# Kernel tuning notes

Hardware: AMD Instinct MI355X
Metric: run time of the kernel (lower is better)

Reference implementation:

```python
import jax, jax.numpy as jnp
import numpy as np

N = 16384      # total ligand atoms
E = 65536      # edges
B = 256        # graphs / batch
MAXN = 64      # atoms per graph (max_nodes for to_dense_batch)
FIN = 64       # num_node_features
HID = 256      # hidden_channels
GH = 2         # gat heads
LP = 1024      # protein length
NH = 4         # cross-attention heads
HD = HID // NH
VOCAB = 22


def setup_inputs() -> dict:
    key = jax.random.key(0)
    ks = jax.random.split(key, 48)
    f = jnp.float32
    def nrm(k, shape, s=0.05):
        return jax.random.normal(k, shape, f) * s
    inp = {}
    inp["x"] = jax.random.normal(ks[0], (N, FIN), f)
    inp["edge_index"] = jax.random.randint(ks[1], (2, E), 0, N)
    inp["batch"] = jnp.arange(N) // MAXN  # sorted, 64 atoms per graph
    inp["protein_seq"] = jax.random.randint(ks[2], (B, LP), 0, VOCAB)
    # GAT layer 1 (FIN -> HID, GH heads, concat=False)
    inp["w1"] = nrm(ks[3], (FIN, GH * HID)); inp["as1"] = nrm(ks[4], (GH, HID)); inp["ad1"] = nrm(ks[5], (GH, HID)); inp["b1"] = jnp.zeros((HID,), f)
    inp["w2"] = nrm(ks[6], (HID, GH * HID)); inp["as2"] = nrm(ks[7], (GH, HID)); inp["ad2"] = nrm(ks[8], (GH, HID)); inp["b2"] = jnp.zeros((HID,), f)
    inp["w3"] = nrm(ks[9], (HID, GH * HID)); inp["as3"] = nrm(ks[10], (GH, HID)); inp["ad3"] = nrm(ks[11], (GH, HID)); inp["b3"] = jnp.zeros((HID,), f)
    # protein embedding + conv1d (OIH layout)
    inp["emb"] = nrm(ks[12], (VOCAB, HID), 0.1)
    inp["conv_w"] = nrm(ks[13], (HID, HID, 3)); inp["conv_b"] = jnp.zeros((HID,), f)
    # cross-attention MHA
    inp["wq"] = nrm(ks[14], (HID, HID)); inp["bq"] = jnp.zeros((HID,), f)
    inp["wk"] = nrm(ks[15], (HID, HID)); inp["bk"] = jnp.zeros((HID,), f)
    inp["wv"] = nrm(ks[16], (HID, HID)); inp["bv"] = jnp.zeros((HID,), f)
    inp["wo"] = nrm(ks[17], (HID, HID)); inp["bo"] = jnp.zeros((HID,), f)
    inp["ln1_g"] = jnp.ones((HID,), f); inp["ln1_b"] = jnp.zeros((HID,), f)
    inp["ffw1"] = nrm(ks[18], (HID, 4 * HID)); inp["ffb1"] = jnp.zeros((4 * HID,), f)
    inp["ffw2"] = nrm(ks[19], (4 * HID, HID)); inp["ffb2"] = jnp.zeros((HID,), f)
    inp["ln2_g"] = jnp.ones((HID,), f); inp["ln2_b"] = jnp.zeros((HID,), f)
    inp["fc1_w"] = nrm(ks[20], (HID, HID)); inp["fc1_b"] = jnp.zeros((HID,), f)
    inp["fc2_w"] = nrm(ks[21], (HID, 1)); inp["fc2_b"] = jnp.zeros((1,), f)
    return inp


def _gat(x, edge_index, W, a_src, a_dst, bias):
    # PyG GATConv, concat=False (mean over heads), add_self_loops=True
    n = x.shape[0]
    h = (x @ W).reshape(n, GH, HID)                      # [N,GH,C]
    loop = jnp.arange(n)
    src = jnp.concatenate([edge_index[0], loop])
    dst = jnp.concatenate([edge_index[1], loop])
    a_s = jnp.einsum('nhc,hc->nh', h, a_src)             # [N,GH]
    a_d = jnp.einsum('nhc,hc->nh', h, a_dst)
    e = jax.nn.leaky_relu(a_s[src] + a_d[dst], 0.2)      # [E+N,GH]
    emax = jax.ops.segment_max(e, dst, num_segments=n)   # each node has a self-loop
    ex = jnp.exp(e - emax[dst])
    den = jax.ops.segment_sum(ex, dst, num_segments=n)
    alpha = ex / den[dst]                                # [E+N,GH]
    msg = h[src] * alpha[:, :, None]
    out = jax.ops.segment_sum(msg, dst, num_segments=n)  # [N,GH,C]
    return out.mean(axis=1) + bias


def _to_dense_batch(x, batch):
    # batch is sorted node->graph ids; counts per graph <= MAXN
    ones = jnp.ones((x.shape[0],), jnp.int32)
    counts = jax.ops.segment_sum(ones, batch, num_segments=B)
    starts = jnp.cumsum(counts) - counts
    pos = jnp.arange(x.shape[0]) - starts[batch]
    dense = jnp.zeros((B, MAXN, x.shape[1]), x.dtype).at[batch, pos].set(x)
    mask = jnp.zeros((B, MAXN), bool).at[batch, pos].set(True)
    return dense, mask


def _layernorm(x, g, b, eps=1e-5):
    mu = x.mean(-1, keepdims=True)
    var = ((x - mu) ** 2).mean(-1, keepdims=True)
    return (x - mu) * jax.lax.rsqrt(var + eps) * g + b


def reference(x, edge_index, batch, protein_seq,
              w1, as1, ad1, b1, w2, as2, ad2, b2, w3, as3, ad3, b3,
              emb, conv_w, conv_b,
              wq, bq, wk, bk, wv, bv, wo, bo,
              ln1_g, ln1_b, ffw1, ffb1, ffw2, ffb2, ln2_g, ln2_b,
              fc1_w, fc1_b, fc2_w, fc2_b):
    # --- ligand GNN (eval mode: dropout = identity) ---
    h = jax.nn.elu(_gat(x, edge_index, w1, as1, ad1, b1))
    h = jax.nn.elu(_gat(h, edge_index, w2, as2, ad2, b2))
    h = jax.nn.elu(_gat(h, edge_index, w3, as3, ad3, b3))
    lig, lig_mask = _to_dense_batch(h, batch)            # [B,MAXN,HID], [B,MAXN]
    # --- protein branch ---
    p = emb[protein_seq]                                 # [B,LP,HID]
    p = p.transpose(0, 2, 1)                             # [B,HID,LP]
    p = jax.lax.conv_general_dilated(p, conv_w, (1,), [(1, 1)],
                                     dimension_numbers=('NCH', 'OIH', 'NCH'))
    p = jax.nn.relu(p + conv_b[None, :, None]).transpose(0, 2, 1)  # [B,LP,HID]
    kpm = protein_seq == 0                               # key padding mask
    # --- cross attention (query=ligand, key/value=protein) ---
    q = (lig @ wq + bq).reshape(B, MAXN, NH, HD)
    k = (p @ wk + bk).reshape(B, LP, NH, HD)
    v = (p @ wv + bv).reshape(B, LP, NH, HD)
    scores = jnp.einsum('bqhd,bkhd->bhqk', q, k) / np.sqrt(HD).astype(np.float32)
    scores = jnp.where(kpm[:, None, None, :], jnp.float32(-1e9), scores)
    attn = jax.nn.softmax(scores, axis=-1)               # [B,NH,MAXN,LP]
    ctx = jnp.einsum('bhqk,bkhd->bqhd', attn, v).reshape(B, MAXN, HID)
    attn_out = ctx @ wo + bo
    y = _layernorm(lig + attn_out, ln1_g, ln1_b)
    ff = jax.nn.gelu(y @ ffw1 + ffb1, approximate=False) @ ffw2 + ffb2
    y = _layernorm(y + ff, ln2_g, ln2_b)
    # --- masked mean pool ---
    m = lig_mask[:, :, None].astype(y.dtype)
    pooled = (y * m).sum(axis=1) / (m.sum(axis=1) + 1e-6)
    out = jax.nn.relu(pooled @ fc1_w + fc1_b)
    return out @ fc2_w + fc2_b                           # [B,1]
```

## Files before the change

### kernel.cpp

```cpp
#include <hip/hip_runtime.h>
#include <hip/hip_bf16.h>
#include <cstdint>
#include <cstddef>

#define NAT 16384
#define NED 65536
#define BGR 256
#define FIN 64
#define HID 256
#define LPN 1024
#define HD 64
#define NTRIP 11638
#define NTAB  11648

typedef __bf16 bf16x8 __attribute__((ext_vector_type(8)));
typedef float floatx4 __attribute__((ext_vector_type(4)));

__device__ __forceinline__ void gl2lds16(const void* g, void* l)
{
    __builtin_amdgcn_global_load_lds(
        (const __attribute__((address_space(1))) unsigned int*)g,
        (__attribute__((address_space(3))) unsigned int*)l, 16, 0, 0);
}

template<int ACT, int OUTBF16, int BIASROW, int HSPLIT>
__global__ __launch_bounds__(512) void gemm_mfma(const __bf16* __restrict__ A,
    const __bf16* __restrict__ Bt, const float* __restrict__ bias,
    void* __restrict__ Cout, int M, int Nn, int K, float escale)
{
    __shared__ __bf16 As[2][128][32];
    __shared__ __bf16 Bs[2][128][32];
    const int t = threadIdx.x;
    const int m0 = blockIdx.y * 128, n0 = blockIdx.x * 128;
    const int w = t >> 6, lane = t & 63;
    const int wm = (w & 3) * 32, wn = (w >> 2) * 64;
    const int quad = lane >> 4, l16 = lane & 15;
    const int r0 = t >> 2, s0 = t & 3, g0 = (s0 ^ (r0 & 3)) * 8;
    const int fso = (quad ^ (l16 & 3)) * 8;
    floatx4 acc[2][4] = {};
    for (int k0 = 0; k0 < K; k0 += 64) {
        gl2lds16(A + (size_t)(m0 + r0) * K + k0 + g0,       &As[0][r0][s0 * 8]);
        gl2lds16(A + (size_t)(m0 + r0) * K + k0 + 32 + g0,  &As[1][r0][s0 * 8]);
        gl2lds16(Bt + (size_t)(n0 + r0) * K + k0 + g0,      &Bs[0][r0][s0 * 8]);
        gl2lds16(Bt + (size_t)(n0 + r0) * K + k0 + 32 + g0, &Bs[1][r0][s0 * 8]);
        __syncthreads();
#pragma unroll
        for (int c = 0; c < 2; c++) {
            bf16x8 af[2], bfr[4];
#pragma unroll
            for (int mi = 0; mi < 2; mi++) af[mi]  = *(const bf16x8*)&As[c][wm + mi * 16 + l16][fso];
#pragma unroll
            for (int nj = 0; nj < 4; nj++) bfr[nj] = *(const bf16x8*)&Bs[c][wn + nj * 16 + l16][fso];
#pragma unroll
            for (int mi = 0; mi < 2; mi++)
#pragma unroll
                for (int nj = 0; nj < 4; nj++)
                    acc[mi][nj] = __builtin_amdgcn_mfma_f32_16x16x32_bf16(af[mi], bfr[nj], acc[mi][nj], 0, 0, 0);
        }
        __syncthreads();
    }
#pragma unroll
    for (int mi = 0; mi < 2; mi++)
#pragma unroll
        for (int nj = 0; nj < 4; nj++) {
            int col = n0 + wn + nj * 16 + l16;
#pragma unroll
            for (int r = 0; r < 4; r++) {
                int row = m0 + wm + mi * 16 + quad * 4 + r;
                float bval = bias ? (BIASROW ? bias[row] : bias[col]) : 0.f;
                float v = (acc[mi][nj][r] + bval) * escale;
                if (ACT == 1) v = fmaxf(v, 0.f);
                if (ACT == 2) v = 0.5f * v * (1.f + erff(v * 0.70710678118654752f));
                if (HSPLIT)      ((__bf16*)Cout)[((size_t)(col >> 6) * M + row) * 64 + (col & 63)] = (__bf16)v;
                else if (OUTBF16) ((__bf16*)Cout)[(size_t)row * Nn + col] = (__bf16)v;
                else              ((float*)Cout)[(size_t)row * Nn + col] = v;
            }
        }
}

__global__ __launch_bounds__(512) void ffn_k(const __bf16* __restrict__ A,
    const __bf16* __restrict__ W1t, const __bf16* __restrict__ W2t,
    const float* __restrict__ b1, const float* __restrict__ b2,
    float* __restrict__ Cout)
{
    __shared__ __bf16 As[64 * 256];
    __shared__ __bf16 Hs[64 * 128];
    const int t = threadIdx.x;
    const int m0 = blockIdx.x * 64;
    const int w = t >> 6, lane = t & 63;
    const int rg = w & 1, cg = w >> 1;
    const int quad = lane >> 4, l16 = lane & 15;
#pragma unroll
    for (int it = 0; it < 4; it++) {
        const int idx = it * 512 + t;
        const int row = idx >> 5, cs = idx & 31;
        const int c = (cs & 24) | ((cs & 7) ^ (row & 7));
        gl2lds16(A + (size_t)(m0 + row) * 256 + c * 8, &As[idx * 8]);
    }
    floatx4 acc2[2][4] = {};
    __syncthreads();
    const int arow0 = rg * 32 + l16;
    for (int ch = 0; ch < 8; ch++) {
        floatx4 acc1[2][2] = {};
#pragma unroll
        for (int w32 = 0; w32 < 8; w32++) {
            bf16x8 a[2];
#pragma unroll
            for (int mi = 0; mi < 2; mi++) {
                const int row = arow0 + mi * 16;
                const int c = w32 * 4 + quad;
                const int slot = (c & 24) | ((c & 7) ^ (row & 7));
                a[mi] = *(const bf16x8*)&As[row * 256 + slot * 8];
            }
#pragma unroll
            for (int nj = 0; nj < 2; nj++) {
                const int hcol = ch * 128 + cg * 32 + nj * 16 + l16;
                bf16x8 bfrag = *(const bf16x8*)(W1t + (size_t)hcol * 256 + w32 * 32 + quad * 8);
#pragma unroll
                for (int mi = 0; mi < 2; mi++)
                    acc1[mi][nj] = __builtin_amdgcn_mfma_f32_16x16x32_bf16(a[mi], bfrag, acc1[mi][nj], 0, 0, 0);
            }
        }
#pragma unroll
        for (int nj = 0; nj < 2; nj++) {
            const int col = cg * 32 + nj * 16 + l16;
            const float bv = b1[ch * 128 + col];
            const int ch8 = col >> 3;
#pragma unroll
            for (int mi = 0; mi < 2; mi++)
#pragma unroll
                for (int r = 0; r < 4; r++) {
                    const int row = rg * 32 + mi * 16 + quad * 4 + r;
                    float v = acc1[mi][nj][r] + bv;
                    v = 0.5f * v * (1.f + erff(v * 0.70710678118654752f));
                    const int slot = (ch8 & 8) | ((ch8 & 7) ^ (row & 7));
                    Hs[row * 128 + slot * 8 + (col & 7)] = (__bf16)v;
                }
        }
        __syncthreads();
#pragma unroll
        for (int ks = 0; ks < 4; ks++) {
            bf16x8 a[2];
#pragma unroll
            for (int mi = 0; mi < 2; mi++) {
                const int row = arow0 + mi * 16;
                const int c8 = ks * 4 + quad;
                const int slot = (c8 & 8) | ((c8 & 7) ^ (row & 7));
                a[mi] = *(const bf16x8*)&Hs[row * 128 + slot * 8];
            }
#pragma unroll
            for (int nj = 0; nj < 4; nj++) {
                const int ocol = cg * 64 + nj * 16 + l16;
                bf16x8 bfrag = *(const bf16x8*)(W2t + (size_t)ocol * 1024 + ch * 128 + ks * 32 + quad * 8);
#pragma unroll
                for (int mi = 0; mi < 2; mi++)
                    acc2[mi][nj] = __builtin_amdgcn_mfma_f32_16x16x32_bf16(a[mi], bfrag, acc2[mi][nj], 0, 0, 0);
            }
        }
        __syncthreads();
    }
#pragma unroll
    for (int mi = 0; mi < 2; mi++)
#pragma unroll
        for (int nj = 0; nj < 4; nj++) {
            const int col = cg * 64 + nj * 16 + l16;
            const float bv = b2[col];
#pragma unroll
            for (int r = 0; r < 4; r++) {
                const int row = m0 + rg * 32 + mi * 16 + quad * 4 + r;
                Cout[(size_t)row * 256 + col] = acc2[mi][nj][r] + bv;
            }
        }
}

__global__ __launch_bounds__(512) void gemm_gat(const __bf16* __restrict__ A,
    const __bf16* __restrict__ Bt, const float* __restrict__ as_f,
    const float* __restrict__ ad_f, __bf16* __restrict__ Hg,
    float* __restrict__ part, int K)
{
    __shared__ __bf16 As[2][128][32];
    __shared__ __bf16 Bs[2][128][32];
    const int t = threadIdx.x;
    const int m0 = blockIdx.y * 128, n0 = blockIdx.x * 128;
    const int w = t >> 6, lane = t & 63;
    const int wm = (w & 3) * 32, wn = (w >> 2) * 64;
    const int quad = lane >> 4, l16 = lane & 15;
    const int r0 = t >> 2, s0 = t & 3, g0 = (s0 ^ (r0 & 3)) * 8;
    const int fso = (quad ^ (l16 & 3)) * 8;
    floatx4 acc[2][4] = {};
    for (int k0 = 0; k0 < K; k0 += 64) {
        gl2lds16(A + (size_t)(m0 + r0) * K + k0 + g0,       &As[0][r0][s0 * 8]);
        gl2lds16(A + (size_t)(m0 + r0) * K + k0 + 32 + g0,  &As[1][r0][s0 * 8]);
        gl2lds16(Bt + (size_t)(n0 + r0) * K + k0 + g0,      &Bs[0][r0][s0 * 8]);
        gl2lds16(Bt + (size_t)(n0 + r0) * K + k0 + 32 + g0, &Bs[1][r0][s0 * 8]);
        __syncthreads();
#pragma unroll
        for (int c = 0; c < 2; c++) {
            bf16x8 af[2], bfr[4];
#pragma unroll
            for (int mi = 0; mi < 2; mi++) af[mi]  = *(const bf16x8*)&As[c][wm + mi * 16 + l16][fso];
#pragma unroll
            for (int nj = 0; nj < 4; nj++) bfr[nj] = *(const bf16x8*)&Bs[c][wn + nj * 16 + l16][fso];
#pragma unroll
            for (int mi = 0; mi < 2; mi++)
#pragma unroll
                for (int nj = 0; nj < 4; nj++)
                    acc[mi][nj] = __builtin_amdgcn_mfma_f32_16x16x32_bf16(af[mi], bfr[nj], acc[mi][nj], 0, 0, 0);
        }
        __syncthreads();
    }
    const int slot = blockIdx.x * 2 + (w >> 2);
#pragma unroll
    for (int mi = 0; mi < 2; mi++) {
#pragma unroll
        for (int r = 0; r < 4; r++) {
            float ps = 0.f, pd = 0.f;
#pragma unroll
            for (int nj = 0; nj < 4; nj++) {
                int col = n0 + wn + nj * 16 + l16;
                float v = acc[mi][nj][r];
                ps += v * as_f[col];
                pd += v * ad_f[col];
            }
#pragma unroll
            for (int off = 1; off < 16; off <<= 1) {
                ps += __shfl_xor(ps, off, 64);
                pd += __shfl_xor(pd, off, 64);
            }
            if (l16 == 0) {
                int row = m0 + wm + mi * 16 + quad * 4 + r;
                part[(size_t)(slot * 2 + 0) * NAT + row] = ps;
                part[(size_t)(slot * 2 + 1) * NAT + row] = pd;
            }
        }
    }
#pragma unroll
    for (int mi = 0; mi < 2; mi++)
#pragma unroll
        for (int nj = 0; nj < 4; nj++) {
            int col = n0 + wn + nj * 16 + l16;
#pragma unroll
            for (int r = 0; r < 4; r++) {
                int row = m0 + wm + mi * 16 + quad * 4 + r;
                Hg[(size_t)row * 512 + col] = (__bf16)acc[mi][nj][r];
            }
        }
}

__global__ void fold_k(const float* __restrict__ part, float* __restrict__ a_s,
                       float* __restrict__ a_d)
{
    int n = blockIdx.x * 256 + threadIdx.x;
    float s0 = 0.f, d0 = 0.f, s1 = 0.f, d1 = 0.f;
#pragma unroll
    for (int sl = 0; sl < 4; sl++) {
        s0 += part[(size_t)(sl * 2 + 0) * NAT + n];
        d0 += part[(size_t)(sl * 2 + 1) * NAT + n];
        s1 += part[(size_t)((sl + 4) * 2 + 0) * NAT + n];
        d1 += part[(size_t)((sl + 4) * 2 + 1) * NAT + n];
    }
    a_s[n * 2 + 0] = s0; a_s[n * 2 + 1] = s1;
    a_d[n * 2 + 0] = d0; a_d[n * 2 + 1] = d1;
}

__global__ __launch_bounds__(256) void tap_k(const float* __restrict__ emb,
    const float* __restrict__ cw, float* __restrict__ tap)
{
    const int dlv = blockIdx.x >> 2, part = blockIdx.x & 3;
    const int dl = dlv / 22, v = dlv % 22;
    const int n = threadIdx.x;
    const float* er = emb + v * 256 + part * 64;
    const float* wr = cw + (size_t)n * 768 + part * 192 + dl;
    float s = 0.f;
    for (int k = 0; k < 64; k += 4) {
        s += er[k + 0] * wr[k * 3 + 0];
        s += er[k + 1] * wr[k * 3 + 3];
        s += er[k + 2] * wr[k * 3 + 6];
        s += er[k + 3] * wr[k * 3 + 9];
    }
    atomicAdd(&tap[(size_t)dlv * 256 + n], s);
}

__global__ __launch_bounds__(256) void ptab_k(const float* __restrict__ tap,
    const float* __restrict__ bias, __bf16* __restrict__ P)
{
    const int t = threadIdx.x;
    const int row = blockIdx.x * 8 + (t >> 5);
    const int c = (t & 31) * 8;
    __bf16 o[8];
    if (row < NTRIP) {
        const int a = row / 506, rem = row - a * 506;
        const int t1 = rem / 23, c2 = rem - t1 * 23;
        float acc[8];
#pragma unroll
        for (int j = 0; j < 8; j++) acc[j] = bias[c + j];
        if (a > 0) {
            const float* r = tap + (size_t)(0 * 22 + (a - 1)) * 256 + c;
#pragma unroll
            for (int j = 0; j < 8; j++) acc[j] += r[j];
        }
        {
            const float* r = tap + (size_t)(1 * 22 + t1) * 256 + c;
#pragma unroll
            for (int j = 0; j < 8; j++) acc[j] += r[j];
        }
        if (c2 > 0) {
            const float* r = tap + (size_t)(2 * 22 + (c2 - 1)) * 256 + c;
#pragma unroll
            for (int j = 0; j < 8; j++) acc[j] += r[j];
        }
#pragma unroll
        for (int j = 0; j < 8; j++) o[j] = (__bf16)fmaxf(acc[j], 0.f);
    } else {
#pragma unroll
        for (int j = 0; j < 8; j++) o[j] = (__bf16)0.f;
    }
    *(uint4*)(P + (size_t)row * 256 + c) = *(uint4*)o;
}

__global__ void tid_k(const int* __restrict__ seq, unsigned short* __restrict__ tid)
{
    int i = blockIdx.x * 256 + threadIdx.x;
    int b = i >> 10, l = i & 1023;
    const int* sr = seq + b * LPN;
    int t0 = (l > 0) ? sr[l - 1] : -1;
    int t1 = sr[l];
    int t2 = (l < LPN - 1) ? sr[l + 1] : -1;
    int v = (t0 + 1) * 506 + t1 * 23 + (t2 + 1);
    tid[i] = (unsigned short)(v | (t1 == 0 ? 0x8000 : 0));
}

struct Segs {
    const float* src[12];
    __bf16* dst[12];
    int kdim[12];
    int ndim[12];
    int mode[12];
    int start[13];
};

__global__ void cvtall_k(Segs S, int total)
{
    int i = blockIdx.x * 256 + threadIdx.x;
    if (i >= total) return;
    int s = 0;
    while (i >= S.start[s + 1]) s++;
    int j = i - S.start[s];
    if (S.mode[s] == 0) {
        S.dst[s][j] = (__bf16)S.src[s][j];
    } else {
        int K = S.kdim[s], N = S.ndim[s];
        int n = j / K, k = j - n * K;
        S.dst[s][j] = (__bf16)S.src[s][(size_t)k * N + n];
    }
}

__global__ void deg_k(const int* __restrict__ ei, int* __restrict__ deg)
{
    int e = blockIdx.x * 256 + threadIdx.x;
    if (e < NED) atomicAdd(&deg[ei[NED + e]], 1);
}

__global__ __launch_bounds__(256) void scan_k(const int* __restrict__ deg, int* __restrict__ rowptr)
{
    __shared__ int part[256];
    int t = threadIdx.x;
    int base = t * 64;
    int s = 0;
#pragma unroll
    for (int i = 0; i < 64; i++) s += deg[base + i];
    part[t] = s;
    __syncthreads();
    for (int off = 1; off < 256; off <<= 1) {
        int v = (t >= off) ? part[t - off] : 0;
        __syncthreads();
        part[t] += v;
        __syncthreads();
    }
    int run = t ? part[t - 1] : 0;
    for (int i = 0; i < 64; i++) { rowptr[base + i] = run; run += deg[base + i]; }
    if (t == 255) rowptr[16384] = run;
}

__global__ void scat_k(const int* __restrict__ ei, int* __restrict__ fill,
                       const int* __restrict__ rowptr, int* __restrict__ csrc,
                       int* __restrict__ cdst)
{
    int e = blockIdx.x * 256 + threadIdx.x;
    if (e >= NED) return;
    int d = ei[NED + e];
    int pos = rowptr[d] + atomicAdd(&fill[d], 1);
    csrc[pos] = ei[e];
    cdst[pos] = d;
}

__global__ void erec_k(const int* __restrict__ csrc, const int* __restrict__ cdst,
    const float* __restrict__ a_s, const float* __restrict__ a_d,
    float4* __restrict__ rec)
{
    int p = blockIdx.x * 256 + threadIdx.x;
    if (p >= NED) return;
    int s = csrc[p], d = cdst[p];
    float2 as2 = *(const float2*)(a_s + s * 2);
    float2 ad2 = *(const float2*)(a_d + d * 2);
    float e0 = as2.x + ad2.x; e0 = (e0 > 0.f) ? e0 : 0.2f * e0;
    float e1 = as2.y + ad2.y; e1 = (e1 > 0.f) ? e1 : 0.2f * e1;
    rec[p] = make_float4(e0, e1, __int_as_float(s), 0.f);
}

__global__ __launch_bounds__(256) void gat_agg(const int* __restrict__ rowptr,
    const float4* __restrict__ rec, const __bf16* __restrict__ hgb,
    const float* __restrict__ a_s, const float* __restrict__ a_d,
    const float* __restrict__ bias, float* __restrict__ out, __bf16* __restrict__ outb)
{
    const int wave = threadIdx.x >> 6, lane = threadIdx.x & 63;
    const int d = blockIdx.x * 4 + wave;
    const int beg = rowptr[d], end = rowptr[d + 1];
    float2 as2 = *(const float2*)(a_s + d * 2);
    float2 ad2 = *(const float2*)(a_d + d * 2);
    float e0 = as2.x + ad2.x; e0 = (e0 > 0.f) ? e0 : 0.2f * e0;
    float e1 = as2.y + ad2.y; e1 = (e1 > 0.f) ? e1 : 0.2f * e1;
    float m0 = e0, den0 = 1.f, m1 = e1, den1 = 1.f;
    for (int p = beg; p < end; p++) {
        float4 rc = rec[p];
        float nm0 = fmaxf(m0, rc.x);
        den0 = den0 * __expf(m0 - nm0) + __expf(rc.x - nm0);
        m0 = nm0;
        float nm1 = fmaxf(m1, rc.y);
        den1 = den1 * __expf(m1 - nm1) + __expf(rc.y - nm1);
        m1 = nm1;
    }
    const float inv0 = 1.f / den0, inv1 = 1.f / den1;
    const int ch = lane * 8;
    const int g = ch >> 8;
    const float mg = g ? m1 : m0, invg = g ? inv1 : inv0;
    float acc[8] = {};
    {
        float al = __expf((g ? e1 : e0) - mg) * invg;
        bf16x8 hv = *(const bf16x8*)(hgb + (size_t)d * 512 + ch);
#pragma unroll
        for (int j = 0; j < 8; j++) acc[j] += (float)hv[j] * al;
    }
    for (int p = beg; p < end; p++) {
        float4 rc = rec[p];
        float al = __expf((g ? rc.y : rc.x) - mg) * invg;
        int s = __float_as_int(rc.z);
        bf16x8 hv = *(const bf16x8*)(hgb + (size_t)s * 512 + ch);
#pragma unroll
        for (int j = 0; j < 8; j++) acc[j] += (float)hv[j] * al;
    }
    float other[8];
#pragma unroll
    for (int j = 0; j < 8; j++) other[j] = __shfl_xor(acc[j], 32, 64);
    if (lane < 32) {
#pragma unroll
        for (int j = 0; j < 8; j++) {
            float v = 0.5f * (acc[j] + other[j]) + bias[ch + j];
            v = (v > 0.f) ? v : expm1f(v);
            if (out) out[(size_t)d * 256 + ch + j] = v;
            outb[(size_t)d * 256 + ch + j] = (__bf16)v;
        }
    }
}

__global__ __launch_bounds__(256, 4) void attn6_k(const __bf16* __restrict__ Qb,
    const __bf16* __restrict__ Ktab, const __bf16* __restrict__ Vtab,
    const unsigned short* __restrict__ tid16, __bf16* __restrict__ O)
{
    __shared__ __bf16 Ks[2][4096];
    __shared__ __bf16 Vs[4096];
    __shared__ __bf16 Ps2[4][16][64];
    __shared__ float mask_f[1024];
    __shared__ unsigned short tids[1024];
    const int t = threadIdx.x;
    const int bid = blockIdx.x;
    const int h = (bid >> 1) & 3;
    const int b = ((bid >> 3) << 1) | (bid & 1);
    const int w = t >> 6, lane = t & 63;
    const int quad = lane >> 4, l16 = lane & 15;
    const int key = (l16 & 7) << 4;
    const __bf16* Kh = Ktab + (size_t)h * NTAB * 64;
    const __bf16* Vh = Vtab + (size_t)h * NTAB * 64;
    {
        const uint32_t* src = (const uint32_t*)(tid16 + (size_t)b * LPN);
        uint32_t v0 = src[t], v1 = src[t + 256];
        ((uint32_t*)tids)[t] = v0;
        ((uint32_t*)tids)[t + 256] = v1;
        mask_f[2 * t + 0] = (v0 & 0x8000u) ? -1e9f : 0.f;
        mask_f[2 * t + 1] = (v0 & 0x80000000u) ? -1e9f : 0.f;
        mask_f[2 * (t + 256) + 0] = (v1 & 0x8000u) ? -1e9f : 0.f;
        mask_f[2 * (t + 256) + 1] = (v1 & 0x80000000u) ? -1e9f : 0.f;
    }
    const __bf16* qrow = Qb + (size_t)(b * 64 + w * 16 + l16) * HID + h * HD;
    bf16x8 aq0 = *(const bf16x8*)(qrow + quad * 8);
    bf16x8 aq1 = *(const bf16x8*)(qrow + 32 + quad * 8);
    __syncthreads();

    auto stageK = [&](int kt, int bufb) {
#pragma unroll
        for (int it = 0; it < 2; it++) {
            const int s = it * 256 + t;
            const int pos = s >> 3;
            const int c = (s & 7) ^ (pos & 7);
            const int row = tids[kt * 64 + pos] & 0x7fff;
            gl2lds16(Kh + (size_t)row * 64 + c * 8,
                     &Ks[bufb][(it * 256 + w * 64) * 8]);
        }
    };
    auto loadV = [&](int kt, bf16x8* vrr) {
#pragma unroll
        for (int it = 0; it < 2; it++) {
            const int pos = w * 8 + (lane >> 3) + it * 32;
            const int row = tids[kt * 64 + pos] & 0x7fff;
            vrr[it] = *(const bf16x8*)(Vh + (size_t)row * 64 + (lane & 7) * 8);
        }
    };
    auto writeV = [&](const bf16x8* vrr) {
        const int p = lane >> 3, c = lane & 7;
#pragma unroll
        for (int it = 0; it < 2; it++) {
            const int pos = w * 8 + p + it * 32;
            const int cp = pos >> 3;
#pragma unroll
            for (int j = 0; j < 8; j++) {
                const int chl = c * 8 + j;
                Vs[chl * 64 + (((cp ^ c ^ j) & 7) << 3) + p] = vrr[it][j];
            }
        }
    };

    bf16x8 vr[2];
    stageK(0, 0);
    loadV(0, vr);
    writeV(vr);
    float m_run = -3e38f;
    float l_run = 0.f;
    floatx4 ctx[4] = {};
    __syncthreads();

    for (int kt = 0; kt < 16; kt++) {
        const int buf = kt & 1;
        const int kp0 = kt * 64;
        if (kt < 15) {
            stageK(kt + 1, buf ^ 1);
            loadV(kt + 1, vr);
        }
        const int ksl0 = (quad ^ (l16 & 7)) * 8;
        const int ksl1 = ((quad + 4) ^ (l16 & 7)) * 8;
        floatx4 s[4];
#pragma unroll
        for (int nj = 0; nj < 4; nj++) {
            const __bf16* kr = &Ks[buf][(nj * 16 + l16) * 64];
            bf16x8 k0 = *(const bf16x8*)&kr[ksl0];
            bf16x8 k1 = *(const bf16x8*)&kr[ksl1];
            floatx4 z = {0.f, 0.f, 0.f, 0.f};
            s[nj] = __builtin_amdgcn_mfma_f32_16x16x32_bf16(k0, aq0, z, 0, 0, 0);
            s[nj] = __builtin_amdgcn_mfma_f32_16x16x32_bf16(k1, aq1, s[nj], 0, 0, 0);
        }
#pragma unroll
        for (int nj = 0; nj < 4; nj++) {
            floatx4 m4 = *(const floatx4*)&mask_f[kp0 + nj * 16 + quad * 4];
#pragma unroll
            for (int r = 0; r < 4; r++) s[nj][r] += m4[r];
        }
        float mx = -3e38f;
#pragma unroll
        for (int nj = 0; nj < 4; nj++)
#pragma unroll
            for (int r = 0; r < 4; r++) mx = fmaxf(mx, s[nj][r]);
        mx = fmaxf(mx, __shfl_xor(mx, 16, 64));
        mx = fmaxf(mx, __shfl_xor(mx, 32, 64));
        const float mn = fmaxf(m_run, mx);
        const float alpha = __expf(m_run - mn);
        m_run = mn;
        float rs = 0.f;
#pragma unroll
        for (int nj = 0; nj < 4; nj++)
#pragma unroll
            for (int r = 0; r < 4; r++) {
                float p = __expf(s[nj][r] - mn);
                s[nj][r] = p;
                rs += p;
            }
        rs += __shfl_xor(rs, 16, 64);
        rs += __shfl_xor(rs, 32, 64);
        l_run = l_run * alpha + rs;
        float al[4];
#pragma unroll
        for (int r = 0; r < 4; r++) al[r] = __shfl(alpha, quad * 4 + r, 64);
        {
            char* rowp = (char*)&Ps2[w][l16][0];
#pragma unroll
            for (int nj = 0; nj < 4; nj++) {
                union { uint2 u2; unsigned short us[4]; } pk;
#pragma unroll
                for (int r = 0; r < 4; r++) {
                    __bf16 bv = (__bf16)s[nj][r];
                    pk.us[r] = *(unsigned short*)&bv;
                }
                *(uint2*)(rowp + ((nj * 32 + quad * 8) ^ key)) = pk.u2;
            }
        }
        bf16x8 pa0 = *(const bf16x8*)((char*)&Ps2[w][l16][0] + ((quad * 16) ^ key));
        bf16x8 pa1 = *(const bf16x8*)((char*)&Ps2[w][l16][0] + ((64 + quad * 16) ^ key));
#pragma unroll
        for (int dj = 0; dj < 4; dj++) {
#pragma unroll
            for (int r = 0; r < 4; r++) ctx[dj][r] *= al[r];
            const int chl = dj * 16 + l16;
            const int Xc = ((chl >> 3) ^ (chl & 7)) & 7;
            bf16x8 bv0 = *(const bf16x8*)&Vs[chl * 64 + (((quad ^ Xc) & 7) << 3)];
            bf16x8 bv1 = *(const bf16x8*)&Vs[chl * 64 + ((((quad + 4) ^ Xc) & 7) << 3)];
            ctx[dj] = __builtin_amdgcn_mfma_f32_16x16x32_bf16(pa0, bv0, ctx[dj], 0, 0, 0);
            ctx[dj] = __builtin_amdgcn_mfma_f32_16x16x32_bf16(pa1, bv1, ctx[dj], 0, 0, 0);
        }
        __syncthreads();
        if (kt < 15) writeV(vr);
        __syncthreads();
    }
    float ll[4];
#pragma unroll
    for (int r = 0; r < 4; r++) ll[r] = __shfl(l_run, quad * 4 + r, 64);
#pragma unroll
    for (int dj = 0; dj < 4; dj++)
#pragma unroll
        for (int r = 0; r < 4; r++) {
            int q = w * 16 + quad * 4 + r;
            O[((size_t)(b * 64 + q)) * 256 + h * HD + dj * 16 + l16] = (__bf16)(ctx[dj][r] / ll[r]);
        }
}

__device__ __forceinline__ float blockSum256(float v, float* red)
{
#pragma unroll
    for (int off = 32; off >= 1; off >>= 1) v += __shfl_down(v, off, 64);
    int wave = threadIdx.x >> 6, lane = threadIdx.x & 63;
    if (lane == 0) red[wave] = v;
    __syncthreads();
    float s = red[0] + red[1] + red[2] + red[3];
    __syncthreads();
    return s;
}

__global__ __launch_bounds__(256) void lnres_k(const float* __restrict__ A,
    const float* __restrict__ Bb, const float* __restrict__ g,
    const float* __restrict__ be, float* __restrict__ Y, __bf16* __restrict__ Yb)
{
    __shared__ float red[4];
    int r = blockIdx.x, t = threadIdx.x;
    float v = A[(size_t)r * 256 + t] + Bb[(size_t)r * 256 + t];
    float mean = blockSum256(v, red) * (1.f / 256.f);
    float d = v - mean;
    float var = blockSum256(d * d, red) * (1.f / 256.f);
    float o = d * rsqrtf(var + 1e-5f) * g[t] + be[t];
    Y[(size_t)r * 256 + t] = o;
    if (Yb) Yb[(size_t)r * 256 + t] = (__bf16)o;
}

__global__ __launch_bounds__(256) void head_k(const float* __restrict__ Y,
    const float* __restrict__ fc1w, const float* __restrict__ fc1b,
    const float* __restrict__ fc2w, const float* __restrict__ fc2b,
    float* __restrict__ out)
{
    __shared__ float pooled[256];
    __shared__ float h[256];
    __shared__ float red[4];
    int b = blockIdx.x, t = threadIdx.x;
    float s = 0.f;
#pragma unroll 8
    for (int q = 0; q < 64; q++) s += Y[(size_t)(b * 64 + q) * 256 + t];
    pooled[t] = s / (64.f + 1e-6f);
    __syncthreads();
    float a = 0.f;
    for (int k = 0; k < 256; k += 4) {
        a += pooled[k + 0] * fc1w[(k + 0) * 256 + t];
        a += pooled[k + 1] * fc1w[(k + 1) * 256 + t];
        a += pooled[k + 2] * fc1w[(k + 2) * 256 + t];
        a += pooled[k + 3] * fc1w[(k + 3) * 256 + t];
    }
    h[t] = fmaxf(a + fc1b[t], 0.f);
    __syncthreads();
    float p = h[t] * fc2w[t];
    p = blockSum256(p, red);
    if (t == 0) out[b] = p + fc2b[0];
}

extern "C" void kernel_launch(void* const* d_in, const int* in_sizes, int n_in,
                              void* d_out, int out_size, void* d_ws, size_t ws_size,
                              hipStream_t stream)
{
    const float* x     = (const float*)d_in[0];
    const int*   ei    = (const int*)d_in[1];
    const int*   pseq  = (const int*)d_in[3];
    const float* w1  = (const float*)d_in[4];
    const float* as1 = (const float*)d_in[5];
    const float* ad1 = (const float*)d_in[6];
    const float* b1  = (const float*)d_in[7];
    const float* w2  = (const float*)d_in[8];
    const float* as2 = (const float*)d_in[9];
    const float* ad2 = (const float*)d_in[10];
    const float* b2  = (const float*)d_in[11];
    const float* w3  = (const float*)d_in[12];
    const float* as3 = (const float*)d_in[13];
    const float* ad3 = (const float*)d_in[14];
    const float* b3  = (const float*)d_in[15];
    const float* emb    = (const float*)d_in[16];
    const float* conv_w = (const float*)d_in[17];
    const float* conv_b = (const float*)d_in[18];
    const float* wq = (const float*)d_in[19];
    const float* bq = (const float*)d_in[20];
    const float* wk = (const float*)d_in[21];
    const float* bk = (const float*)d_in[22];
    const float* wv = (const float*)d_in[23];
    const float* bv = (const float*)d_in[24];
    const float* wo = (const float*)d_in[25];
    const float* bo = (const float*)d_in[26];
    const float* ln1_g = (const float*)d_in[27];
    const float* ln1_b = (const float*)d_in[28];
    const float* ffw1  = (const float*)d_in[29];
    const float* ffb1  = (const float*)d_in[30];
    const float* ffw2  = (const float*)d_in[31];
    const float* ffb2  = (const float*)d_in[32];
    const float* ln2_g = (const float*)d_in[33];
    const float* ln2_b = (const float*)d_in[34];
    const float* fc1_w = (const float*)d_in[35];
    const float* fc1_b = (const float*)d_in[36];
    const float* fc2_w = (const float*)d_in[37];
    const float* fc2_b = (const float*)d_in[38];
    (void)in_sizes; (void)n_in; (void)out_size;

    char* ws = (char*)d_ws;
    size_t off = 0;
    auto alloc = [&](size_t bytes) -> char* {
        char* p = ws + off;
        off += (bytes + 255) & ~(size_t)255;
        return p;
    };
    __bf16* hgb  = (__bf16*)alloc((size_t)NAT * 512 * 2);
    float* og    = (float*)alloc((size_t)NAT * 512 * 4);
    float* hb0   = (float*)alloc((size_t)NAT * 256 * 4);
    float* hb1   = (float*)alloc((size_t)NAT * 256 * 4);
    __bf16* xb   = (__bf16*)alloc((size_t)NAT * FIN * 2);
    __bf16* hbb  = (__bf16*)alloc((size_t)NAT * 256 * 2);
    __bf16* qbb  = (__bf16*)alloc((size_t)NAT * 256 * 2);
    __bf16* ctxbb= (__bf16*)alloc((size_t)NAT * 256 * 2);
    __bf16* ybb  = (__bf16*)alloc((size_t)NAT * 256 * 2);
    float* a_s   = (float*)alloc((size_t)NAT * 2 * 4);
    float* a_d   = (float*)alloc((size_t)NAT * 2 * 4);
    float* asd_p = (float*)alloc((size_t)16 * NAT * 4);
    int* deg     = (int*)alloc((size_t)NAT * 4);
    int* fill    = (int*)alloc((size_t)NAT * 4);
    int* rowptr  = (int*)alloc((size_t)(NAT + 1) * 4);
    int* csrc    = (int*)alloc((size_t)NED * 4);
    int* cdst    = (int*)alloc((size_t)NED * 4);
    float4* erec = (float4*)alloc((size_t)NED * 16);
    float* tap   = (float*)alloc((size_t)3 * 22 * 256 * 4);
    __bf16* ptab = (__bf16*)alloc((size_t)NTAB * 256 * 2);
    __bf16* Ktab = (__bf16*)alloc((size_t)NTAB * 256 * 2);
    __bf16* Vtab = (__bf16*)alloc((size_t)NTAB * 256 * 2);
    unsigned short* tid16 = (unsigned short*)alloc((size_t)BGR * LPN * 2);
    __bf16* w1T  = (__bf16*)alloc((size_t)512 * 64 * 2);
    __bf16* w2T  = (__bf16*)alloc((size_t)512 * 256 * 2);
    __bf16* w3T  = (__bf16*)alloc((size_t)512 * 256 * 2);
    __bf16* wkT  = (__bf16*)alloc((size_t)256 * 256 * 2);
    __bf16* wvT  = (__bf16*)alloc((size_t)256 * 256 * 2);
    __bf16* wqT  = (__bf16*)alloc((size_t)256 * 256 * 2);
    __bf16* woT  = (__bf16*)alloc((size_t)256 * 256 * 2);
    __bf16* f1T  = (__bf16*)alloc((size_t)1024 * 256 * 2);
    __bf16* f2T  = (__bf16*)alloc((size_t)256 * 1024 * 2);
    size_t fixed_end = off;
    char* region   = ws + fixed_end;
    float*  y2     = (float*)(region + (size_t)NAT * 1024 * 2);
    float* attno = og;
    float* ybuf  = og + (size_t)NAT * 256;
    float* ff2o  = hb1;
    (void)ws_size;

    hipMemsetAsync(deg, 0, (size_t)NAT * 8, stream);
    hipMemsetAsync(tap, 0, (size_t)3 * 22 * 256 * 4, stream);
    deg_k<<<NED / 256, 256, 0, stream>>>(ei, deg);
    scan_k<<<1, 256, 0, stream>>>(deg, rowptr);
    scat_k<<<NED / 256, 256, 0, stream>>>(ei, fill, rowptr, csrc, cdst);
    tap_k<<<264, 256, 0, stream>>>(emb, conv_w, tap);

    {
        Segs S;
        const float* srcs[10] = {x, w1, w2, w3, wk, wv, wq, wo, ffw1, ffw2};
        __bf16* dsts[10] = {xb, w1T, w2T, w3T, wkT, wvT, wqT, woT, f1T, f2T};
        int kd[10] = {0, 64, 256, 256, 256, 256, 256, 256, 256, 1024};
        int nd[10] = {0, 512, 512, 512, 256, 256, 256, 256, 1024, 256};
        int md[10] = {0, 1, 1, 1, 1, 1, 1, 1, 1, 1};
        int cnt[10] = {NAT * FIN, 32768, 131072, 131072,
                       65536, 65536, 65536, 65536, 262144, 262144};
        int run = 0;
        for (int i = 0; i < 10; i++) {
            S.src[i] = srcs[i]; S.dst[i] = dsts[i];
            S.kdim[i] = kd[i]; S.ndim[i] = nd[i]; S.mode[i] = md[i];
            S.start[i] = run; run += cnt[i];
        }
        S.start[10] = run; S.start[11] = run; S.start[12] = run;
        cvtall_k<<<(run + 255) / 256, 256, 0, stream>>>(S, run);
    }

    ptab_k<<<NTAB / 8, 256, 0, stream>>>(tap, conv_b, ptab);
    tid_k<<<BGR * LPN / 256, 256, 0, stream>>>(pseq, tid16);
    gemm_mfma<0, 1, 0, 1><<<dim3(2, NTAB / 128), 512, 0, stream>>>(ptab, wkT, bk, Ktab, NTAB, 256, 256, 1.f);
    gemm_mfma<0, 1, 0, 1><<<dim3(2, NTAB / 128), 512, 0, stream>>>(ptab, wvT, bv, Vtab, NTAB, 256, 256, 1.f);

    const __bf16* WT[3] = {w1T, w2T, w3T};
    const float* asl[3] = {as1, as2, as3};
    const float* adl[3] = {ad1, ad2, ad3};
    const float* bl[3]  = {b1, b2, b3};
    float* houts[3] = {nullptr, nullptr, hb0};
    const __bf16* hinb = xb;
    int Kdim = FIN;
    for (int l = 0; l < 3; l++) {
        gemm_gat<<<dim3(4, NAT / 128), 512, 0, stream>>>(hinb, WT[l], asl[l], adl[l], hgb, asd_p, Kdim);
        fold_k<<<NAT / 256, 256, 0, stream>>>(asd_p, a_s, a_d);
        erec_k<<<NED / 256, 256, 0, stream>>>(csrc, cdst, a_s, a_d, erec);
        gat_agg<<<NAT / 4, 256, 0, stream>>>(rowptr, erec, hgb, a_s, a_d, bl[l], houts[l], hbb);
        hinb = hbb;
        Kdim = HID;
    }
    const float* lig = hb0;
    const __bf16* ligb = hbb;

    gemm_mfma<0, 1, 0, 0><<<dim3(2, NAT / 128), 512, 0, stream>>>(ligb, wqT, bq, qbb, NAT, 256, 256, 0.125f);

    attn6_k<<<BGR * 4, 256, 0, stream>>>(qbb, Ktab, Vtab, tid16, ctxbb);

    gemm_mfma<0, 0, 0, 0><<<dim3(2, NAT / 128), 512, 0, stream>>>(ctxbb, woT, bo, attno, NAT, 256, 256, 1.f);
    lnres_k<<<NAT, 256, 0, stream>>>(lig, attno, ln1_g, ln1_b, ybuf, ybb);
    ffn_k<<<NAT / 64, 512, 0, stream>>>(ybb, f1T, f2T, ffb1, ffb2, ff2o);
    lnres_k<<<NAT, 256, 0, stream>>>(ybuf, ff2o, ln2_g, ln2_b, y2, nullptr);

    head_k<<<BGR, 256, 0, stream>>>(y2, fc1_w, fc1_b, fc2_w, fc2_b, (float*)d_out);
}
```

Baseline: 537.3 us.

## Merge K/V table GEMMs into one launch and shrink FFN row tile

```diff
diff --git a/kernel.cpp b/kernel.cpp
--- a/kernel.cpp
+++ b/kernel.cpp
@@ -78,47 +78,94 @@
         }
 }
 
-__global__ __launch_bounds__(512) void ffn_k(const __bf16* __restrict__ A,
+__global__ __launch_bounds__(512) void kvtab_k(const __bf16* __restrict__ A,
+    const __bf16* __restrict__ wkT, const __bf16* __restrict__ wvT,
+    const float* __restrict__ bk, const float* __restrict__ bv,
+    __bf16* __restrict__ Ktab, __bf16* __restrict__ Vtab)
+{
+    __shared__ __bf16 As[2][128][32];
+    __shared__ __bf16 Bs[2][128][32];
+    const int t = threadIdx.x;
+    const int z = blockIdx.x >> 1;
+    const int m0 = blockIdx.y * 128, n0 = (blockIdx.x & 1) * 128;
+    const __bf16* Bt = z ? wvT : wkT;
+    const float* bias = z ? bv : bk;
+    __bf16* Cout = z ? Vtab : Ktab;
+    const int w = t >> 6, lane = t & 63;
+    const int wm = (w & 3) * 32, wn = (w >> 2) * 64;
+    const int quad = lane >> 4, l16 = lane & 15;
+    const int r0 = t >> 2, s0 = t & 3, g0 = (s0 ^ (r0 & 3)) * 8;
+    const int fso = (quad ^ (l16 & 3)) * 8;
+    floatx4 acc[2][4] = {};
+    for (int k0 = 0; k0 < 256; k0 += 64) {
+        gl2lds16(A + (size_t)(m0 + r0) * 256 + k0 + g0,       &As[0][r0][s0 * 8]);
+        gl2lds16(A + (size_t)(m0 + r0) * 256 + k0 + 32 + g0,  &As[1][r0][s0 * 8]);
+        gl2lds16(Bt + (size_t)(n0 + r0) * 256 + k0 + g0,      &Bs[0][r0][s0 * 8]);
+        gl2lds16(Bt + (size_t)(n0 + r0) * 256 + k0 + 32 + g0, &Bs[1][r0][s0 * 8]);
+        __syncthreads();
+#pragma unroll
+        for (int c = 0; c < 2; c++) {
+            bf16x8 af[2], bfr[4];
+#pragma unroll
+            for (int mi = 0; mi < 2; mi++) af[mi]  = *(const bf16x8*)&As[c][wm + mi * 16 + l16][fso];
+#pragma unroll
+            for (int nj = 0; nj < 4; nj++) bfr[nj] = *(const bf16x8*)&Bs[c][wn + nj * 16 + l16][fso];
+#pragma unroll
+            for (int mi = 0; mi < 2; mi++)
+#pragma unroll
+                for (int nj = 0; nj < 4; nj++)
+                    acc[mi][nj] = __builtin_amdgcn_mfma_f32_16x16x32_bf16(af[mi], bfr[nj], acc[mi][nj], 0, 0, 0);
+        }
+        __syncthreads();
+    }
+#pragma unroll
+    for (int mi = 0; mi < 2; mi++)
+#pragma unroll
+        for (int nj = 0; nj < 4; nj++) {
+            int col = n0 + wn + nj * 16 + l16;
+#pragma unroll
+            for (int r = 0; r < 4; r++) {
+                int row = m0 + wm + mi * 16 + quad * 4 + r;
+                float v = acc[mi][nj][r] + bias[col];
+                Cout[((size_t)(col >> 6) * NTAB + row) * 64 + (col & 63)] = (__bf16)v;
+            }
+        }
+}
+
+__global__ __launch_bounds__(512, 4) void ffn2_k(const __bf16* __restrict__ A,
     const __bf16* __restrict__ W1t, const __bf16* __restrict__ W2t,
     const float* __restrict__ b1, const float* __restrict__ b2,
     float* __restrict__ Cout)
 {
-    __shared__ __bf16 As[64 * 256];
-    __shared__ __bf16 Hs[64 * 128];
+    __shared__ __bf16 As[32 * 256];
+    __shared__ __bf16 Hs[2][32 * 128];
     const int t = threadIdx.x;
-    const int m0 = blockIdx.x * 64;
+    const int m0 = blockIdx.x * 32;
     const int w = t >> 6, lane = t & 63;
     const int rg = w & 1, cg = w >> 1;
     const int quad = lane >> 4, l16 = lane & 15;
 #pragma unroll
-    for (int it = 0; it < 4; it++) {
+    for (int it = 0; it < 2; it++) {
         const int idx = it * 512 + t;
         const int row = idx >> 5, cs = idx & 31;
         const int c = (cs & 24) | ((cs & 7) ^ (row & 7));
         gl2lds16(A + (size_t)(m0 + row) * 256 + c * 8, &As[idx * 8]);
     }
-    floatx4 acc2[2][4] = {};
+    floatx4 acc2[4] = {};
     __syncthreads();
-    const int arow0 = rg * 32 + l16;
+    const int arow = rg * 16 + l16;
     for (int ch = 0; ch < 8; ch++) {
-        floatx4 acc1[2][2] = {};
+        floatx4 acc1[2] = {};
 #pragma unroll
         for (int w32 = 0; w32 < 8; w32++) {
-            bf16x8 a[2];
-#pragma unroll
-            for (int mi = 0; mi < 2; mi++) {
-                const int row = arow0 + mi * 16;
-                const int c = w32 * 4 + quad;
-                const int slot = (c & 24) | ((c & 7) ^ (row & 7));
-                a[mi] = *(const bf16x8*)&As[row * 256 + slot * 8];
-            }
+            const int c = w32 * 4 + quad;
+            const int slot = (c & 24) | ((c & 7) ^ (arow & 7));
+            bf16x8 a = *(const bf16x8*)&As[arow * 256 + slot * 8];
 #pragma unroll
             for (int nj = 0; nj < 2; nj++) {
                 const int hcol = ch * 128 + cg * 32 + nj * 16 + l16;
                 bf16x8 bfrag = *(const bf16x8*)(W1t + (size_t)hcol * 256 + w32 * 32 + quad * 8);
-#pragma unroll
-                for (int mi = 0; mi < 2; mi++)
-                    acc1[mi][nj] = __builtin_amdgcn_mfma_f32_16x16x32_bf16(a[mi], bfrag, acc1[mi][nj], 0, 0, 0);
+                acc1[nj] = __builtin_amdgcn_mfma_f32_16x16x32_bf16(a, bfrag, acc1[nj], 0, 0, 0);
             }
         }
 #pragma unroll
@@ -127,50 +174,38 @@
             const float bv = b1[ch * 128 + col];
             const int ch8 = col >> 3;
 #pragma unroll
-            for (int mi = 0; mi < 2; mi++)
-#pragma unroll
-                for (int r = 0; r < 4; r++) {
-                    const int row = rg * 32 + mi * 16 + quad * 4 + r;
-                    float v = acc1[mi][nj][r] + bv;
-                    v = 0.5f * v * (1.f + erff(v * 0.70710678118654752f));
-                    const int slot = (ch8 & 8) | ((ch8 & 7) ^ (row & 7));
-                    Hs[row * 128 + slot * 8 + (col & 7)] = (__bf16)v;
-                }
+            for (int r = 0; r < 4; r++) {
+                const int row = rg * 16 + quad * 4 + r;
+                float v = acc1[nj][r] + bv;
+                v = 0.5f * v * (1.f + erff(v * 0.70710678118654752f));
+                const int slot = (ch8 & 8) | ((ch8 & 7) ^ (row & 7));
+                Hs[ch & 1][row * 128 + slot * 8 + (col & 7)] = (__bf16)v;
+            }
         }
         __syncthreads();
 #pragma unroll
         for (int ks = 0; ks < 4; ks++) {
-            bf16x8 a[2];
-#pragma unroll
-            for (int mi = 0; mi < 2; mi++) {
-                const int row = arow0 + mi * 16;
-                const int c8 = ks * 4 + quad;
-                const int slot = (c8 & 8) | ((c8 & 7) ^ (row & 7));
-                a[mi] = *(const bf16x8*)&Hs[row * 128 + slot * 8];
-            }
+            const int c8 = ks * 4 + quad;
+            const int slot = (c8 & 8) | ((c8 & 7) ^ (arow & 7));
+            bf16x8 a = *(const bf16x8*)&Hs[ch & 1][arow * 128 + slot * 8];
 #pragma unroll
             for (int nj = 0; nj < 4; nj++) {
                 const int ocol = cg * 64 + nj * 16 + l16;
                 bf16x8 bfrag = *(const bf16x8*)(W2t + (size_t)ocol * 1024 + ch * 128 + ks * 32 + quad * 8);
-#pragma unroll
-                for (int mi = 0; mi < 2; mi++)
-                    acc2[mi][nj] = __builtin_amdgcn_mfma_f32_16x16x32_bf16(a[mi], bfrag, acc2[mi][nj], 0, 0, 0);
-            }
-        }
-        __syncthreads();
-    }
-#pragma unroll
-    for (int mi = 0; mi < 2; mi++)
-#pragma unroll
-        for (int nj = 0; nj < 4; nj++) {
-            const int col = cg * 64 + nj * 16 + l16;
-            const float bv = b2[col];
-#pragma unroll
-            for (int r = 0; r < 4; r++) {
-                const int row = m0 + rg * 32 + mi * 16 + quad * 4 + r;
-                Cout[(size_t)row * 256 + col] = acc2[mi][nj][r] + bv;
-            }
-        }
+                acc2[nj] = __builtin_amdgcn_mfma_f32_16x16x32_bf16(a, bfrag, acc2[nj], 0, 0, 0);
+            }
+        }
+    }
+#pragma unroll
+    for (int nj = 0; nj < 4; nj++) {
+        const int col = cg * 64 + nj * 16 + l16;
+        const float bv = b2[col];
+#pragma unroll
+        for (int r = 0; r < 4; r++) {
+            const int row = m0 + rg * 16 + quad * 4 + r;
+            Cout[(size_t)row * 256 + col] = acc2[nj][r] + bv;
+        }
+    }
 }
 
 __global__ __launch_bounds__(512) void gemm_gat(const __bf16* __restrict__ A,
@@ -804,8 +839,7 @@
 
     ptab_k<<<NTAB / 8, 256, 0, stream>>>(tap, conv_b, ptab);
     tid_k<<<BGR * LPN / 256, 256, 0, stream>>>(pseq, tid16);
-    gemm_mfma<0, 1, 0, 1><<<dim3(2, NTAB / 128), 512, 0, stream>>>(ptab, wkT, bk, Ktab, NTAB, 256, 256, 1.f);
-    gemm_mfma<0, 1, 0, 1><<<dim3(2, NTAB / 128), 512, 0, stream>>>(ptab, wvT, bv, Vtab, NTAB, 256, 256, 1.f);
+    kvtab_k<<<dim3(4, NTAB / 128), 512, 0, stream>>>(ptab, wkT, wvT, bk, bv, Ktab, Vtab);
 
     const __bf16* WT[3] = {w1T, w2T, w3T};
     const float* asl[3] = {as1, as2, as3};
@@ -831,7 +865,7 @@
 
     gemm_mfma<0, 0, 0, 0><<<dim3(2, NAT / 128), 512, 0, stream>>>(ctxbb, woT, bo, attno, NAT, 256, 256, 1.f);
     lnres_k<<<NAT, 256, 0, stream>>>(lig, attno, ln1_g, ln1_b, ybuf, ybb);
-    ffn_k<<<NAT / 64, 512, 0, stream>>>(ybb, f1T, f2T, ffb1, ffb2, ff2o);
+    ffn2_k<<<NAT / 32, 512, 0, stream>>>(ybb, f1T, f2T, ffb1, ffb2, ff2o);
     lnres_k<<<NAT, 256, 0, stream>>>(ybuf, ff2o, ln2_g, ln2_b, y2, nullptr);
 
     head_k<<<BGR, 256, 0, stream>>>(y2, fc1_w, fc1_b, fc2_w, fc2_b, (float*)d_out);
```

Measured after the change: 558.1 us. 3.9% more time.
